# Kernel optimization log

Hardware: AMD Instinct MI355X
Metric: run time of the kernel (lower is better)

Reference implementation:

```python
import jax, jax.numpy as jnp
import numpy as np

N, D, E = 50000, 64, 800000


def setup_inputs() -> dict:
    key = jax.random.key(0)
    ks = jax.random.split(key, 12)
    scale = 1.0 / np.sqrt(D)
    inp = {
        "edge_emb_eq1": jax.random.normal(ks[0], (N, D), dtype=jnp.float32),
        "edge_index": jax.random.randint(ks[1], (2, E), 0, N, dtype=jnp.int64),
    }
    names = ["W1", "b1", "W2", "b2", "Ws", "bs", "Wmu", "bmu", "Wlv", "blv"]
    for i, name in enumerate(names):
        if name.startswith("W"):
            inp[name] = jax.random.normal(ks[2 + i], (D, D), dtype=jnp.float32) * scale
        else:
            inp[name] = jnp.zeros((D,), dtype=jnp.float32)
    return inp


def _gcn(x, W, b, src, dst, dinv):
    # GCNConv: linear transform, then symmetric-normalized aggregation with self-loops.
    x = x @ W  # [N, D]
    coef = dinv[src] * dinv[dst]                      # [E]
    msg = x[src] * coef[:, None]                      # gather + scale, [E, D]
    agg = jax.ops.segment_sum(msg, dst, num_segments=x.shape[0])  # scatter-add
    agg = agg + x * (dinv * dinv)[:, None]            # self-loop contribution
    return agg + b


def reference(edge_emb_eq1, edge_index, W1, b1, W2, b2, Ws, bs, Wmu, bmu, Wlv, blv):
    src, dst = edge_index[0], edge_index[1]
    n = edge_emb_eq1.shape[0]
    # degree (with self-loops) from destination nodes, as in PyG GCNConv
    deg = jax.ops.segment_sum(jnp.ones_like(dst, dtype=edge_emb_eq1.dtype), dst, num_segments=n) + 1.0
    dinv = jax.lax.rsqrt(deg)

    x = edge_emb_eq1
    x = _gcn(x, W1, b1, src, dst, dinv)   # encoder layer 0 (.flatten(1) is a no-op on 2D)
    x = _gcn(x, W2, b2, src, dst, dinv)   # encoder layer 1
    x = jax.nn.relu(_gcn(x, Ws, bs, src, dst, dinv))
    mu = _gcn(x, Wmu, bmu, src, dst, dinv)
    logvar = _gcn(x, Wlv, blv, src, dst, dinv)
    return (mu, logvar)
```

## Files before the change

kernel.cpp:

```cpp
#include <hip/hip_runtime.h>

#define D 64

__global__ void k_zero4(float4* __restrict__ p, int n4) {
    int i = blockIdx.x * 256 + threadIdx.x;
    if (i < n4) p[i] = make_float4(0.f, 0.f, 0.f, 0.f);
}

__global__ void k_deg(const int* __restrict__ dst, int* __restrict__ cnt8,
                      int* __restrict__ rank, int N, int E) {
    int e = blockIdx.x * 256 + threadIdx.x;
    if (e < E) rank[e] = atomicAdd(&cnt8[(size_t)(blockIdx.x & 7) * N + dst[e]], 1);
}

__global__ void k_scan1(const int* __restrict__ cnt8, int* __restrict__ part, int N) {
    __shared__ int s[256];
    int t = threadIdx.x;
    int i = blockIdx.x * 256 + t;
    int v = 0;
    if (i < N) {
        #pragma unroll
        for (int c = 0; c < 8; ++c) v += cnt8[(size_t)c * N + i];
    }
    s[t] = (v + 7) & ~7;
    __syncthreads();
    for (int d = 128; d > 0; d >>= 1) {
        if (t < d) s[t] += s[t + d];
        __syncthreads();
    }
    if (t == 0) part[blockIdx.x] = s[0];
}

__global__ void k_scan2(const int* __restrict__ part, int* __restrict__ boff, int nb) {
    __shared__ int s[256];
    int t = threadIdx.x;
    int v = (t < nb) ? part[t] : 0;
    s[t] = v;
    __syncthreads();
    for (int d = 1; d < 256; d <<= 1) {
        int add = (t >= d) ? s[t - d] : 0;
        __syncthreads();
        s[t] += add;
        __syncthreads();
    }
    if (t < nb) boff[t] = s[t] - v;
}

__global__ void k_scan3(const int* __restrict__ cnt8, const int* __restrict__ boff,
                        int* __restrict__ rp, int* __restrict__ off8,
                        float* __restrict__ dinv, int N) {
    __shared__ int s[256];
    int t = threadIdx.x;
    int i = blockIdx.x * 256 + t;
    int vc[8];
    int v = 0;
    if (i < N) {
        #pragma unroll
        for (int c = 0; c < 8; ++c) { vc[c] = cnt8[(size_t)c * N + i]; v += vc[c]; }
    }
    int pv = (v + 7) & ~7;
    s[t] = pv;
    __syncthreads();
    for (int d = 1; d < 256; d <<= 1) {
        int add = (t >= d) ? s[t - d] : 0;
        __syncthreads();
        s[t] += add;
        __syncthreads();
    }
    if (i < N) {
        int excl = boff[blockIdx.x] + s[t] - pv;
        rp[i] = excl;
        dinv[i] = 1.0f / sqrtf((float)v + 1.0f);
        int run = excl;
        #pragma unroll
        for (int c = 0; c < 8; ++c) { off8[(size_t)c * N + i] = run; run += vc[c]; }
        if (i == N - 1) rp[N] = excl + pv;
    }
}

__global__ void k_fill(const int* __restrict__ src, const int* __restrict__ dst,
                       const int* __restrict__ rank, const int* __restrict__ off8,
                       const float* __restrict__ dinv, int2* __restrict__ pack,
                       int N, int E) {
    int e = blockIdx.x * 256 + threadIdx.x;
    if (e < E) {
        int s = src[e];
        int2 p;
        p.x = s;
        p.y = __float_as_int(dinv[s]);
        pack[off8[(size_t)(blockIdx.x & 7) * N + dst[e]] + rank[e]] = p;
    }
}

template <int RELU>
__global__ __launch_bounds__(256) void k_fused(const float* __restrict__ x,
                                               const int* __restrict__ rp,
                                               const int* __restrict__ packi,
                                               const float* __restrict__ dinv,
                                               const float* __restrict__ W,
                                               const float* __restrict__ b,
                                               float* __restrict__ y, int N) {
    __shared__ float Wl[D * D];
    __shared__ float zs[16][68];
    int t = threadIdx.x;

    #pragma unroll
    for (int r = 0; r < 4; ++r) {
        float4 wv = reinterpret_cast<const float4*>(W)[t + 256 * r];
        *reinterpret_cast<float4*>(&Wl[(t + 256 * r) * 4]) = wv;
    }

    int lane = t & 63;
    int g = lane >> 4;
    int l16 = lane & 15;
    int r_loc = (t >> 6) * 4 + g;
    int n = blockIdx.x * 16 + r_loc;
    if (n < N) {
        int s0 = rp[n], s1 = rp[n + 1];
        float dn = dinv[n];
        const float4* x4 = reinterpret_cast<const float4*>(x);
        const int4* pk = reinterpret_cast<const int4*>(packi);
        float4 sv = x4[(size_t)n * 16 + l16];
        float dnn = dn * dn;
        float ax = sv.x * dnn, ay = sv.y * dnn, az = sv.z * dnn, aw = sv.w * dnn;
        float bx = 0.f, by = 0.f, bz = 0.f, bw = 0.f;
        int e = s0;
        int4 q0, q1, q2, q3;
        if (e < s1) {
            int h = e >> 1;
            q0 = pk[h]; q1 = pk[h + 1]; q2 = pk[h + 2]; q3 = pk[h + 3];
        }
        while (e < s1) {
            float4 v0 = x4[(size_t)q0.x * 16 + l16];
            float4 v1 = x4[(size_t)q0.z * 16 + l16];
            float4 v2 = x4[(size_t)q1.x * 16 + l16];
            float4 v3 = x4[(size_t)q1.z * 16 + l16];
            float4 v4 = x4[(size_t)q2.x * 16 + l16];
            float4 v5 = x4[(size_t)q2.z * 16 + l16];
            float4 v6 = x4[(size_t)q3.x * 16 + l16];
            float4 v7 = x4[(size_t)q3.z * 16 + l16];
            float c0 = __int_as_float(q0.y) * dn, c1 = __int_as_float(q0.w) * dn;
            float c2 = __int_as_float(q1.y) * dn, c3 = __int_as_float(q1.w) * dn;
            float c4 = __int_as_float(q2.y) * dn, c5 = __int_as_float(q2.w) * dn;
            float c6 = __int_as_float(q3.y) * dn, c7 = __int_as_float(q3.w) * dn;
            e += 8;
            if (e < s1) {
                int h = e >> 1;
                q0 = pk[h]; q1 = pk[h + 1]; q2 = pk[h + 2]; q3 = pk[h + 3];
            }
            ax = fmaf(v0.x, c0, ax); ay = fmaf(v0.y, c0, ay); az = fmaf(v0.z, c0, az); aw = fmaf(v0.w, c0, aw);
            bx = fmaf(v1.x, c1, bx); by = fmaf(v1.y, c1, by); bz = fmaf(v1.z, c1, bz); bw = fmaf(v1.w, c1, bw);
            ax = fmaf(v2.x, c2, ax); ay = fmaf(v2.y, c2, ay); az = fmaf(v2.z, c2, az); aw = fmaf(v2.w, c2, aw);
            bx = fmaf(v3.x, c3, bx); by = fmaf(v3.y, c3, by); bz = fmaf(v3.z, c3, bz); bw = fmaf(v3.w, c3, bw);
            ax = fmaf(v4.x, c4, ax); ay = fmaf(v4.y, c4, ay); az = fmaf(v4.z, c4, az); aw = fmaf(v4.w, c4, aw);
            bx = fmaf(v5.x, c5, bx); by = fmaf(v5.y, c5, by); bz = fmaf(v5.z, c5, bz); bw = fmaf(v5.w, c5, bw);
            ax = fmaf(v6.x, c6, ax); ay = fmaf(v6.y, c6, ay); az = fmaf(v6.z, c6, az); aw = fmaf(v6.w, c6, aw);
            bx = fmaf(v7.x, c7, bx); by = fmaf(v7.y, c7, by); bz = fmaf(v7.z, c7, bz); bw = fmaf(v7.w, c7, bw);
        }
        *reinterpret_cast<float4*>(&zs[r_loc][l16 * 4]) =
            make_float4(ax + bx, ay + by, az + bz, aw + bw);
    }
    __syncthreads();

    int col4 = (t & 15) * 4;
    int row = t >> 4;
    int nn = blockIdx.x * 16 + row;
    if (nn < N) {
        float4 acc = make_float4(0.f, 0.f, 0.f, 0.f);
        #pragma unroll
        for (int k = 0; k < D; k += 4) {
            float4 zv = *reinterpret_cast<const float4*>(&zs[row][k]);
            float4 w0 = *reinterpret_cast<const float4*>(&Wl[(k + 0) * D + col4]);
            float4 w1 = *reinterpret_cast<const float4*>(&Wl[(k + 1) * D + col4]);
            float4 w2 = *reinterpret_cast<const float4*>(&Wl[(k + 2) * D + col4]);
            float4 w3 = *reinterpret_cast<const float4*>(&Wl[(k + 3) * D + col4]);
            acc.x = fmaf(zv.x, w0.x, acc.x); acc.y = fmaf(zv.x, w0.y, acc.y);
            acc.z = fmaf(zv.x, w0.z, acc.z); acc.w = fmaf(zv.x, w0.w, acc.w);
            acc.x = fmaf(zv.y, w1.x, acc.x); acc.y = fmaf(zv.y, w1.y, acc.y);
            acc.z = fmaf(zv.y, w1.z, acc.z); acc.w = fmaf(zv.y, w1.w, acc.w);
            acc.x = fmaf(zv.z, w2.x, acc.x); acc.y = fmaf(zv.z, w2.y, acc.y);
            acc.z = fmaf(zv.z, w2.z, acc.z); acc.w = fmaf(zv.z, w2.w, acc.w);
            acc.x = fmaf(zv.w, w3.x, acc.x); acc.y = fmaf(zv.w, w3.y, acc.y);
            acc.z = fmaf(zv.w, w3.z, acc.z); acc.w = fmaf(zv.w, w3.w, acc.w);
        }
        float4 bv = *reinterpret_cast<const float4*>(&b[col4]);
        float4 r = make_float4(acc.x + bv.x, acc.y + bv.y, acc.z + bv.z, acc.w + bv.w);
        if (RELU) {
            r.x = fmaxf(r.x, 0.f); r.y = fmaxf(r.y, 0.f);
            r.z = fmaxf(r.z, 0.f); r.w = fmaxf(r.w, 0.f);
        }
        *reinterpret_cast<float4*>(&y[(size_t)nn * D + col4]) = r;
    }
}

__global__ __launch_bounds__(256) void k_fused_dual(const float* __restrict__ x,
                                                    const int* __restrict__ rp,
                                                    const int* __restrict__ packi,
                                                    const float* __restrict__ dinv,
                                                    const float* __restrict__ Wa,
                                                    const float* __restrict__ ba,
                                                    const float* __restrict__ Wb,
                                                    const float* __restrict__ bb,
                                                    float* __restrict__ ya,
                                                    float* __restrict__ yb, int N) {
    __shared__ float Wla[D * D];
    __shared__ float Wlb[D * D];
    __shared__ float zs[16][68];
    int t = threadIdx.x;

    #pragma unroll
    for (int r = 0; r < 4; ++r) {
        float4 wv = reinterpret_cast<const float4*>(Wa)[t + 256 * r];
        *reinterpret_cast<float4*>(&Wla[(t + 256 * r) * 4]) = wv;
        float4 wv2 = reinterpret_cast<const float4*>(Wb)[t + 256 * r];
        *reinterpret_cast<float4*>(&Wlb[(t + 256 * r) * 4]) = wv2;
    }

    int lane = t & 63;
    int g = lane >> 4;
    int l16 = lane & 15;
    int r_loc = (t >> 6) * 4 + g;
    int n = blockIdx.x * 16 + r_loc;
    if (n < N) {
        int s0 = rp[n], s1 = rp[n + 1];
        float dn = dinv[n];
        const float4* x4 = reinterpret_cast<const float4*>(x);
        const int4* pk = reinterpret_cast<const int4*>(packi);
        float4 sv = x4[(size_t)n * 16 + l16];
        float dnn = dn * dn;
        float ax = sv.x * dnn, ay = sv.y * dnn, az = sv.z * dnn, aw = sv.w * dnn;
        float bx = 0.f, by = 0.f, bz = 0.f, bw = 0.f;
        int e = s0;
        int4 q0, q1, q2, q3;
        if (e < s1) {
            int h = e >> 1;
            q0 = pk[h]; q1 = pk[h + 1]; q2 = pk[h + 2]; q3 = pk[h + 3];
        }
        while (e < s1) {
            float4 v0 = x4[(size_t)q0.x * 16 + l16];
            float4 v1 = x4[(size_t)q0.z * 16 + l16];
            float4 v2 = x4[(size_t)q1.x * 16 + l16];
            float4 v3 = x4[(size_t)q1.z * 16 + l16];
            float4 v4 = x4[(size_t)q2.x * 16 + l16];
            float4 v5 = x4[(size_t)q2.z * 16 + l16];
            float4 v6 = x4[(size_t)q3.x * 16 + l16];
            float4 v7 = x4[(size_t)q3.z * 16 + l16];
            float c0 = __int_as_float(q0.y) * dn, c1 = __int_as_float(q0.w) * dn;
            float c2 = __int_as_float(q1.y) * dn, c3 = __int_as_float(q1.w) * dn;
            float c4 = __int_as_float(q2.y) * dn, c5 = __int_as_float(q2.w) * dn;
            float c6 = __int_as_float(q3.y) * dn, c7 = __int_as_float(q3.w) * dn;
            e += 8;
            if (e < s1) {
                int h = e >> 1;
                q0 = pk[h]; q1 = pk[h + 1]; q2 = pk[h + 2]; q3 = pk[h + 3];
            }
            ax = fmaf(v0.x, c0, ax); ay = fmaf(v0.y, c0, ay); az = fmaf(v0.z, c0, az); aw = fmaf(v0.w, c0, aw);
            bx = fmaf(v1.x, c1, bx); by = fmaf(v1.y, c1, by); bz = fmaf(v1.z, c1, bz); bw = fmaf(v1.w, c1, bw);
            ax = fmaf(v2.x, c2, ax); ay = fmaf(v2.y, c2, ay); az = fmaf(v2.z, c2, az); aw = fmaf(v2.w, c2, aw);
            bx = fmaf(v3.x, c3, bx); by = fmaf(v3.y, c3, by); bz = fmaf(v3.z, c3, bz); bw = fmaf(v3.w, c3, bw);
            ax = fmaf(v4.x, c4, ax); ay = fmaf(v4.y, c4, ay); az = fmaf(v4.z, c4, az); aw = fmaf(v4.w, c4, aw);
            bx = fmaf(v5.x, c5, bx); by = fmaf(v5.y, c5, by); bz = fmaf(v5.z, c5, bz); bw = fmaf(v5.w, c5, bw);
            ax = fmaf(v6.x, c6, ax); ay = fmaf(v6.y, c6, ay); az = fmaf(v6.z, c6, az); aw = fmaf(v6.w, c6, aw);
            bx = fmaf(v7.x, c7, bx); by = fmaf(v7.y, c7, by); bz = fmaf(v7.z, c7, bz); bw = fmaf(v7.w, c7, bw);
        }
        *reinterpret_cast<float4*>(&zs[r_loc][l16 * 4]) =
            make_float4(ax + bx, ay + by, az + bz, aw + bw);
    }
    __syncthreads();

    int col4 = (t & 15) * 4;
    int row = t >> 4;
    int nn = blockIdx.x * 16 + row;
    if (nn < N) {
        float4 acc = make_float4(0.f, 0.f, 0.f, 0.f);
        float4 acd = make_float4(0.f, 0.f, 0.f, 0.f);
        #pragma unroll
        for (int k = 0; k < D; k += 2) {
            float z0 = zs[row][k], z1 = zs[row][k + 1];
            float4 w0 = *reinterpret_cast<const float4*>(&Wla[(k + 0) * D + col4]);
            float4 w1 = *reinterpret_cast<const float4*>(&Wla[(k + 1) * D + col4]);
            float4 u0 = *reinterpret_cast<const float4*>(&Wlb[(k + 0) * D + col4]);
            float4 u1 = *reinterpret_cast<const float4*>(&Wlb[(k + 1) * D + col4]);
            acc.x = fmaf(z0, w0.x, acc.x); acc.y = fmaf(z0, w0.y, acc.y);
            acc.z = fmaf(z0, w0.z, acc.z); acc.w = fmaf(z0, w0.w, acc.w);
            acc.x = fmaf(z1, w1.x, acc.x); acc.y = fmaf(z1, w1.y, acc.y);
            acc.z = fmaf(z1, w1.z, acc.z); acc.w = fmaf(z1, w1.w, acc.w);
            acd.x = fmaf(z0, u0.x, acd.x); acd.y = fmaf(z0, u0.y, acd.y);
            acd.z = fmaf(z0, u0.z, acd.z); acd.w = fmaf(z0, u0.w, acd.w);
            acd.x = fmaf(z1, u1.x, acd.x); acd.y = fmaf(z1, u1.y, acd.y);
            acd.z = fmaf(z1, u1.z, acd.z); acd.w = fmaf(z1, u1.w, acd.w);
        }
        float4 bav = *reinterpret_cast<const float4*>(&ba[col4]);
        float4 bbv = *reinterpret_cast<const float4*>(&bb[col4]);
        *reinterpret_cast<float4*>(&ya[(size_t)nn * D + col4]) =
            make_float4(acc.x + bav.x, acc.y + bav.y, acc.z + bav.z, acc.w + bav.w);
        *reinterpret_cast<float4*>(&yb[(size_t)nn * D + col4]) =
            make_float4(acd.x + bbv.x, acd.y + bbv.y, acd.z + bbv.z, acd.w + bbv.w);
    }
}

extern "C" void kernel_launch(void* const* d_in, const int* in_sizes, int n_in,
                              void* d_out, int out_size, void* d_ws, size_t ws_size,
                              hipStream_t stream) {
    const float* x0  = (const float*)d_in[0];
    const int*   ei  = (const int*)d_in[1];
    const float* W1  = (const float*)d_in[2];
    const float* b1  = (const float*)d_in[3];
    const float* W2  = (const float*)d_in[4];
    const float* b2  = (const float*)d_in[5];
    const float* Wsc = (const float*)d_in[6];
    const float* bs  = (const float*)d_in[7];
    const float* Wmu = (const float*)d_in[8];
    const float* bmu = (const float*)d_in[9];
    const float* Wlv = (const float*)d_in[10];
    const float* blv = (const float*)d_in[11];

    int N = in_sizes[0] / D;
    int E = in_sizes[1] / 2;
    const int* src = ei;
    const int* dst = ei + E;

    char* ws = (char*)d_ws;
    size_t off = 0;
    auto alloc = [&](size_t bytes) {
        char* p = ws + off;
        off += (bytes + 255) & ~(size_t)255;
        return p;
    };
    int*   rp   = (int*)alloc((size_t)(N + 1) * 4);
    float* dinv = (float*)alloc((size_t)N * 4);
    int NB = (N + 255) / 256;
    int* part = (int*)alloc((size_t)NB * 4);
    int* boff = (int*)alloc((size_t)NB * 4);
    int* rank = (int*)alloc((size_t)E * 4);
    int* off8 = (int*)alloc((size_t)8 * N * 4);
    char* zero_base = ws + off;
    int*  cnt8 = (int*)alloc((size_t)8 * N * 4);
    int2* pack = (int2*)alloc(((size_t)E + 8 * (size_t)N) * 8);
    size_t zero_bytes = (size_t)((char*)(pack + E + 8 * (size_t)N) - zero_base);
    int n4 = (int)((zero_bytes + 15) / 16);
    float* h1 = (float*)alloc((size_t)N * D * 4);
    float* h2 = (float*)alloc((size_t)N * D * 4);

    float* mu = (float*)d_out;
    float* lv = (float*)d_out + (size_t)N * D;

    int EB = (E + 255) / 256;
    k_zero4<<<(n4 + 255) / 256, 256, 0, stream>>>((float4*)zero_base, n4);
    k_deg  <<<EB, 256, 0, stream>>>(dst, cnt8, rank, N, E);
    k_scan1<<<NB, 256, 0, stream>>>(cnt8, part, N);
    k_scan2<<<1, 256, 0, stream>>>(part, boff, NB);
    k_scan3<<<NB, 256, 0, stream>>>(cnt8, boff, rp, off8, dinv, N);
    k_fill <<<EB, 256, 0, stream>>>(src, dst, rank, off8, dinv, pack, N, E);

    int FB = (N + 15) / 16;
    k_fused<0><<<FB, 256, 0, stream>>>(x0, rp, (const int*)pack, dinv, W1, b1, h1, N);
    k_fused<0><<<FB, 256, 0, stream>>>(h1, rp, (const int*)pack, dinv, W2, b2, h2, N);
    k_fused<1><<<FB, 256, 0, stream>>>(h2, rp, (const int*)pack, dinv, Wsc, bs, h1, N);
    k_fused_dual<<<FB, 256, 0, stream>>>(h1, rp, (const int*)pack, dinv,
                                         Wmu, bmu, Wlv, blv, mu, lv, N);
}
```

Baseline: 189.2 us.

## Drop shared-memory weight staging and block barrier; read W from global per row

Stops copying the 64x64 weight matrices into shared memory. The mini-GEMM now reads W directly from global memory, where it should stay cache resident. The block-wide __syncthreads is also removed: each row's 16 lanes, all in one wavefront, write zs and then read back only their own row, so only a wavefront-local dependency remains. This cuts LDS usage from about 20-36KB to about 4KB per block, which raises occupancy for the latency-bound gather and lets finished waves exit early. It also switches the edge-pack loads to nontemporal loads. The cost is repeated global/L1 reads of W per row and reliance on wave-synchronous LDS visibility without an explicit barrier.

```diff
diff --git a/kernel.cpp b/kernel.cpp
--- a/kernel.cpp
+++ b/kernel.cpp
@@ -1,6 +1,13 @@
 #include <hip/hip_runtime.h>
 
 #define D 64
+
+typedef int i32x4 __attribute__((ext_vector_type(4)));
+
+__device__ __forceinline__ int4 nt_load_i4(const int4* p) {
+    i32x4 v = __builtin_nontemporal_load(reinterpret_cast<const i32x4*>(p));
+    return make_int4(v.x, v.y, v.z, v.w);
+}
 
 __global__ void k_zero4(float4* __restrict__ p, int n4) {
     int i = blockIdx.x * 256 + threadIdx.x;
@@ -92,6 +99,51 @@
     }
 }
 
+__device__ __forceinline__ float4 agg_row(const float4* __restrict__ x4,
+                                          const int4* __restrict__ pk,
+                                          int s0, int s1, float dn, int n, int l16) {
+    float4 sv = x4[(size_t)n * 16 + l16];
+    float dnn = dn * dn;
+    float ax = sv.x * dnn, ay = sv.y * dnn, az = sv.z * dnn, aw = sv.w * dnn;
+    float bx = 0.f, by = 0.f, bz = 0.f, bw = 0.f;
+    int e = s0;
+    int4 q0, q1, q2, q3;
+    if (e < s1) {
+        int h = e >> 1;
+        q0 = nt_load_i4(&pk[h + 0]); q1 = nt_load_i4(&pk[h + 1]);
+        q2 = nt_load_i4(&pk[h + 2]); q3 = nt_load_i4(&pk[h + 3]);
+    }
+    while (e < s1) {
+        float4 v0 = x4[(size_t)q0.x * 16 + l16];
+        float4 v1 = x4[(size_t)q0.z * 16 + l16];
+        float4 v2 = x4[(size_t)q1.x * 16 + l16];
+        float4 v3 = x4[(size_t)q1.z * 16 + l16];
+        float4 v4 = x4[(size_t)q2.x * 16 + l16];
+        float4 v5 = x4[(size_t)q2.z * 16 + l16];
+        float4 v6 = x4[(size_t)q3.x * 16 + l16];
+        float4 v7 = x4[(size_t)q3.z * 16 + l16];
+        float c0 = __int_as_float(q0.y) * dn, c1 = __int_as_float(q0.w) * dn;
+        float c2 = __int_as_float(q1.y) * dn, c3 = __int_as_float(q1.w) * dn;
+        float c4 = __int_as_float(q2.y) * dn, c5 = __int_as_float(q2.w) * dn;
+        float c6 = __int_as_float(q3.y) * dn, c7 = __int_as_float(q3.w) * dn;
+        e += 8;
+        if (e < s1) {
+            int h = e >> 1;
+            q0 = nt_load_i4(&pk[h + 0]); q1 = nt_load_i4(&pk[h + 1]);
+            q2 = nt_load_i4(&pk[h + 2]); q3 = nt_load_i4(&pk[h + 3]);
+        }
+        ax = fmaf(v0.x, c0, ax); ay = fmaf(v0.y, c0, ay); az = fmaf(v0.z, c0, az); aw = fmaf(v0.w, c0, aw);
+        bx = fmaf(v1.x, c1, bx); by = fmaf(v1.y, c1, by); bz = fmaf(v1.z, c1, bz); bw = fmaf(v1.w, c1, bw);
+        ax = fmaf(v2.x, c2, ax); ay = fmaf(v2.y, c2, ay); az = fmaf(v2.z, c2, az); aw = fmaf(v2.w, c2, aw);
+        bx = fmaf(v3.x, c3, bx); by = fmaf(v3.y, c3, by); bz = fmaf(v3.z, c3, bz); bw = fmaf(v3.w, c3, bw);
+        ax = fmaf(v4.x, c4, ax); ay = fmaf(v4.y, c4, ay); az = fmaf(v4.z, c4, az); aw = fmaf(v4.w, c4, aw);
+        bx = fmaf(v5.x, c5, bx); by = fmaf(v5.y, c5, by); bz = fmaf(v5.z, c5, bz); bw = fmaf(v5.w, c5, bw);
+        ax = fmaf(v6.x, c6, ax); ay = fmaf(v6.y, c6, ay); az = fmaf(v6.z, c6, az); aw = fmaf(v6.w, c6, aw);
+        bx = fmaf(v7.x, c7, bx); by = fmaf(v7.y, c7, by); bz = fmaf(v7.z, c7, bz); bw = fmaf(v7.w, c7, bw);
+    }
+    return make_float4(ax + bx, ay + by, az + bz, aw + bw);
+}
+
 template <int RELU>
 __global__ __launch_bounds__(256) void k_fused(const float* __restrict__ x,
                                                const int* __restrict__ rp,
@@ -100,97 +152,45 @@
                                                const float* __restrict__ W,
                                                const float* __restrict__ b,
                                                float* __restrict__ y, int N) {
-    __shared__ float Wl[D * D];
     __shared__ float zs[16][68];
     int t = threadIdx.x;
-
-    #pragma unroll
-    for (int r = 0; r < 4; ++r) {
-        float4 wv = reinterpret_cast<const float4*>(W)[t + 256 * r];
-        *reinterpret_cast<float4*>(&Wl[(t + 256 * r) * 4]) = wv;
-    }
-
     int lane = t & 63;
     int g = lane >> 4;
     int l16 = lane & 15;
     int r_loc = (t >> 6) * 4 + g;
     int n = blockIdx.x * 16 + r_loc;
-    if (n < N) {
-        int s0 = rp[n], s1 = rp[n + 1];
-        float dn = dinv[n];
-        const float4* x4 = reinterpret_cast<const float4*>(x);
-        const int4* pk = reinterpret_cast<const int4*>(packi);
-        float4 sv = x4[(size_t)n * 16 + l16];
-        float dnn = dn * dn;
-        float ax = sv.x * dnn, ay = sv.y * dnn, az = sv.z * dnn, aw = sv.w * dnn;
-        float bx = 0.f, by = 0.f, bz = 0.f, bw = 0.f;
-        int e = s0;
-        int4 q0, q1, q2, q3;
-        if (e < s1) {
-            int h = e >> 1;
-            q0 = pk[h]; q1 = pk[h + 1]; q2 = pk[h + 2]; q3 = pk[h + 3];
-        }
-        while (e < s1) {
-            float4 v0 = x4[(size_t)q0.x * 16 + l16];
-            float4 v1 = x4[(size_t)q0.z * 16 + l16];
-            float4 v2 = x4[(size_t)q1.x * 16 + l16];
-            float4 v3 = x4[(size_t)q1.z * 16 + l16];
-            float4 v4 = x4[(size_t)q2.x * 16 + l16];
-            float4 v5 = x4[(size_t)q2.z * 16 + l16];
-            float4 v6 = x4[(size_t)q3.x * 16 + l16];
-            float4 v7 = x4[(size_t)q3.z * 16 + l16];
-            float c0 = __int_as_float(q0.y) * dn, c1 = __int_as_float(q0.w) * dn;
-            float c2 = __int_as_float(q1.y) * dn, c3 = __int_as_float(q1.w) * dn;
-            float c4 = __int_as_float(q2.y) * dn, c5 = __int_as_float(q2.w) * dn;
-            float c6 = __int_as_float(q3.y) * dn, c7 = __int_as_float(q3.w) * dn;
-            e += 8;
-            if (e < s1) {
-                int h = e >> 1;
-                q0 = pk[h]; q1 = pk[h + 1]; q2 = pk[h + 2]; q3 = pk[h + 3];
-            }
-            ax = fmaf(v0.x, c0, ax); ay = fmaf(v0.y, c0, ay); az = fmaf(v0.z, c0, az); aw = fmaf(v0.w, c0, aw);
-            bx = fmaf(v1.x, c1, bx); by = fmaf(v1.y, c1, by); bz = fmaf(v1.z, c1, bz); bw = fmaf(v1.w, c1, bw);
-            ax = fmaf(v2.x, c2, ax); ay = fmaf(v2.y, c2, ay); az = fmaf(v2.z, c2, az); aw = fmaf(v2.w, c2, aw);
-            bx = fmaf(v3.x, c3, bx); by = fmaf(v3.y, c3, by); bz = fmaf(v3.z, c3, bz); bw = fmaf(v3.w, c3, bw);
-            ax = fmaf(v4.x, c4, ax); ay = fmaf(v4.y, c4, ay); az = fmaf(v4.z, c4, az); aw = fmaf(v4.w, c4, aw);
-            bx = fmaf(v5.x, c5, bx); by = fmaf(v5.y, c5, by); bz = fmaf(v5.z, c5, bz); bw = fmaf(v5.w, c5, bw);
-            ax = fmaf(v6.x, c6, ax); ay = fmaf(v6.y, c6, ay); az = fmaf(v6.z, c6, az); aw = fmaf(v6.w, c6, aw);
-            bx = fmaf(v7.x, c7, bx); by = fmaf(v7.y, c7, by); bz = fmaf(v7.z, c7, bz); bw = fmaf(v7.w, c7, bw);
-        }
-        *reinterpret_cast<float4*>(&zs[r_loc][l16 * 4]) =
-            make_float4(ax + bx, ay + by, az + bz, aw + bw);
-    }
-    __syncthreads();
-
-    int col4 = (t & 15) * 4;
-    int row = t >> 4;
-    int nn = blockIdx.x * 16 + row;
-    if (nn < N) {
-        float4 acc = make_float4(0.f, 0.f, 0.f, 0.f);
-        #pragma unroll
-        for (int k = 0; k < D; k += 4) {
-            float4 zv = *reinterpret_cast<const float4*>(&zs[row][k]);
-            float4 w0 = *reinterpret_cast<const float4*>(&Wl[(k + 0) * D + col4]);
-            float4 w1 = *reinterpret_cast<const float4*>(&Wl[(k + 1) * D + col4]);
-            float4 w2 = *reinterpret_cast<const float4*>(&Wl[(k + 2) * D + col4]);
-            float4 w3 = *reinterpret_cast<const float4*>(&Wl[(k + 3) * D + col4]);
-            acc.x = fmaf(zv.x, w0.x, acc.x); acc.y = fmaf(zv.x, w0.y, acc.y);
-            acc.z = fmaf(zv.x, w0.z, acc.z); acc.w = fmaf(zv.x, w0.w, acc.w);
-            acc.x = fmaf(zv.y, w1.x, acc.x); acc.y = fmaf(zv.y, w1.y, acc.y);
-            acc.z = fmaf(zv.y, w1.z, acc.z); acc.w = fmaf(zv.y, w1.w, acc.w);
-            acc.x = fmaf(zv.z, w2.x, acc.x); acc.y = fmaf(zv.z, w2.y, acc.y);
-            acc.z = fmaf(zv.z, w2.z, acc.z); acc.w = fmaf(zv.z, w2.w, acc.w);
-            acc.x = fmaf(zv.w, w3.x, acc.x); acc.y = fmaf(zv.w, w3.y, acc.y);
-            acc.z = fmaf(zv.w, w3.z, acc.z); acc.w = fmaf(zv.w, w3.w, acc.w);
-        }
-        float4 bv = *reinterpret_cast<const float4*>(&b[col4]);
-        float4 r = make_float4(acc.x + bv.x, acc.y + bv.y, acc.z + bv.z, acc.w + bv.w);
-        if (RELU) {
-            r.x = fmaxf(r.x, 0.f); r.y = fmaxf(r.y, 0.f);
-            r.z = fmaxf(r.z, 0.f); r.w = fmaxf(r.w, 0.f);
-        }
-        *reinterpret_cast<float4*>(&y[(size_t)nn * D + col4]) = r;
-    }
+    if (n >= N) return;
+
+    float4 z = agg_row(reinterpret_cast<const float4*>(x),
+                       reinterpret_cast<const int4*>(packi),
+                       rp[n], rp[n + 1], dinv[n], n, l16);
+    *reinterpret_cast<float4*>(&zs[r_loc][l16 * 4]) = z;
+
+    int col4 = l16 * 4;
+    float4 acc = make_float4(0.f, 0.f, 0.f, 0.f);
+    #pragma unroll 4
+    for (int k = 0; k < D; k += 4) {
+        float4 zv = *reinterpret_cast<const float4*>(&zs[r_loc][k]);
+        float4 w0 = *reinterpret_cast<const float4*>(&W[(k + 0) * D + col4]);
+        float4 w1 = *reinterpret_cast<const float4*>(&W[(k + 1) * D + col4]);
+        float4 w2 = *reinterpret_cast<const float4*>(&W[(k + 2) * D + col4]);
+        float4 w3 = *reinterpret_cast<const float4*>(&W[(k + 3) * D + col4]);
+        acc.x = fmaf(zv.x, w0.x, acc.x); acc.y = fmaf(zv.x, w0.y, acc.y);
+        acc.z = fmaf(zv.x, w0.z, acc.z); acc.w = fmaf(zv.x, w0.w, acc.w);
+        acc.x = fmaf(zv.y, w1.x, acc.x); acc.y = fmaf(zv.y, w1.y, acc.y);
+        acc.z = fmaf(zv.y, w1.z, acc.z); acc.w = fmaf(zv.y, w1.w, acc.w);
+        acc.x = fmaf(zv.z, w2.x, acc.x); acc.y = fmaf(zv.z, w2.y, acc.y);
+        acc.z = fmaf(zv.z, w2.z, acc.z); acc.w = fmaf(zv.z, w2.w, acc.w);
+        acc.x = fmaf(zv.w, w3.x, acc.x); acc.y = fmaf(zv.w, w3.y, acc.y);
+        acc.z = fmaf(zv.w, w3.z, acc.z); acc.w = fmaf(zv.w, w3.w, acc.w);
+    }
+    float4 bv = *reinterpret_cast<const float4*>(&b[col4]);
+    float4 r = make_float4(acc.x + bv.x, acc.y + bv.y, acc.z + bv.z, acc.w + bv.w);
+    if (RELU) {
+        r.x = fmaxf(r.x, 0.f); r.y = fmaxf(r.y, 0.f);
+        r.z = fmaxf(r.z, 0.f); r.w = fmaxf(r.w, 0.f);
+    }
+    *reinterpret_cast<float4*>(&y[(size_t)n * D + col4]) = r;
 }
 
 __global__ __launch_bounds__(256) void k_fused_dual(const float* __restrict__ x,
@@ -203,100 +203,45 @@
                                                     const float* __restrict__ bb,
                                                     float* __restrict__ ya,
                                                     float* __restrict__ yb, int N) {
-    __shared__ float Wla[D * D];
-    __shared__ float Wlb[D * D];
     __shared__ float zs[16][68];
     int t = threadIdx.x;
-
-    #pragma unroll
-    for (int r = 0; r < 4; ++r) {
-        float4 wv = reinterpret_cast<const float4*>(Wa)[t + 256 * r];
-        *reinterpret_cast<float4*>(&Wla[(t + 256 * r) * 4]) = wv;
-        float4 wv2 = reinterpret_cast<const float4*>(Wb)[t + 256 * r];
-        *reinterpret_cast<float4*>(&Wlb[(t + 256 * r) * 4]) = wv2;
-    }
-
     int lane = t & 63;
     int g = lane >> 4;
     int l16 = lane & 15;
     int r_loc = (t >> 6) * 4 + g;
     int n = blockIdx.x * 16 + r_loc;
-    if (n < N) {
-        int s0 = rp[n], s1 = rp[n + 1];
-        float dn = dinv[n];
-        const float4* x4 = reinterpret_cast<const float4*>(x);
-        const int4* pk = reinterpret_cast<const int4*>(packi);
-        float4 sv = x4[(size_t)n * 16 + l16];
-        float dnn = dn * dn;
-        float ax = sv.x * dnn, ay = sv.y * dnn, az = sv.z * dnn, aw = sv.w * dnn;
-        float bx = 0.f, by = 0.f, bz = 0.f, bw = 0.f;
-        int e = s0;
-        int4 q0, q1, q2, q3;
-        if (e < s1) {
-            int h = e >> 1;
-            q0 = pk[h]; q1 = pk[h + 1]; q2 = pk[h + 2]; q3 = pk[h + 3];
-        }
-        while (e < s1) {
-            float4 v0 = x4[(size_t)q0.x * 16 + l16];
-            float4 v1 = x4[(size_t)q0.z * 16 + l16];
-            float4 v2 = x4[(size_t)q1.x * 16 + l16];
-            float4 v3 = x4[(size_t)q1.z * 16 + l16];
-            float4 v4 = x4[(size_t)q2.x * 16 + l16];
-            float4 v5 = x4[(size_t)q2.z * 16 + l16];
-            float4 v6 = x4[(size_t)q3.x * 16 + l16];
-            float4 v7 = x4[(size_t)q3.z * 16 + l16];
-            float c0 = __int_as_float(q0.y) * dn, c1 = __int_as_float(q0.w) * dn;
-            float c2 = __int_as_float(q1.y) * dn, c3 = __int_as_float(q1.w) * dn;
-            float c4 = __int_as_float(q2.y) * dn, c5 = __int_as_float(q2.w) * dn;
-            float c6 = __int_as_float(q3.y) * dn, c7 = __int_as_float(q3.w) * dn;
-            e += 8;
-            if (e < s1) {
-                int h = e >> 1;
-                q0 = pk[h]; q1 = pk[h + 1]; q2 = pk[h + 2]; q3 = pk[h + 3];
-            }
-            ax = fmaf(v0.x, c0, ax); ay = fmaf(v0.y, c0, ay); az = fmaf(v0.z, c0, az); aw = fmaf(v0.w, c0, aw);
-            bx = fmaf(v1.x, c1, bx); by = fmaf(v1.y, c1, by); bz = fmaf(v1.z, c1, bz); bw = fmaf(v1.w, c1, bw);
-            ax = fmaf(v2.x, c2, ax); ay = fmaf(v2.y, c2, ay); az = fmaf(v2.z, c2, az); aw = fmaf(v2.w, c2, aw);
-            bx = fmaf(v3.x, c3, bx); by = fmaf(v3.y, c3, by); bz = fmaf(v3.z, c3, bz); bw = fmaf(v3.w, c3, bw);
-            ax = fmaf(v4.x, c4, ax); ay = fmaf(v4.y, c4, ay); az = fmaf(v4.z, c4, az); aw = fmaf(v4.w, c4, aw);
-            bx = fmaf(v5.x, c5, bx); by = fmaf(v5.y, c5, by); bz = fmaf(v5.z, c5, bz); bw = fmaf(v5.w, c5, bw);
-            ax = fmaf(v6.x, c6, ax); ay = fmaf(v6.y, c6, ay); az = fmaf(v6.z, c6, az); aw = fmaf(v6.w, c6, aw);
-            bx = fmaf(v7.x, c7, bx); by = fmaf(v7.y, c7, by); bz = fmaf(v7.z, c7, bz); bw = fmaf(v7.w, c7, bw);
-        }
-        *reinterpret_cast<float4*>(&zs[r_loc][l16 * 4]) =
-            make_float4(ax + bx, ay + by, az + bz, aw + bw);
-    }
-    __syncthreads();
-
-    int col4 = (t & 15) * 4;
-    int row = t >> 4;
-    int nn = blockIdx.x * 16 + row;
-    if (nn < N) {
-        float4 acc = make_float4(0.f, 0.f, 0.f, 0.f);
-        float4 acd = make_float4(0.f, 0.f, 0.f, 0.f);
-        #pragma unroll
-        for (int k = 0; k < D; k += 2) {
-            float z0 = zs[row][k], z1 = zs[row][k + 1];
-            float4 w0 = *reinterpret_cast<const float4*>(&Wla[(k + 0) * D + col4]);
-            float4 w1 = *reinterpret_cast<const float4*>(&Wla[(k + 1) * D + col4]);
-            float4 u0 = *reinterpret_cast<const float4*>(&Wlb[(k + 0) * D + col4]);
-            float4 u1 = *reinterpret_cast<const float4*>(&Wlb[(k + 1) * D + col4]);
-            acc.x = fmaf(z0, w0.x, acc.x); acc.y = fmaf(z0, w0.y, acc.y);
-            acc.z = fmaf(z0, w0.z, acc.z); acc.w = fmaf(z0, w0.w, acc.w);
-            acc.x = fmaf(z1, w1.x, acc.x); acc.y = fmaf(z1, w1.y, acc.y);
-            acc.z = fmaf(z1, w1.z, acc.z); acc.w = fmaf(z1, w1.w, acc.w);
-            acd.x = fmaf(z0, u0.x, acd.x); acd.y = fmaf(z0, u0.y, acd.y);
-            acd.z = fmaf(z0, u0.z, acd.z); acd.w = fmaf(z0, u0.w, acd.w);
-            acd.x = fmaf(z1, u1.x, acd.x); acd.y = fmaf(z1, u1.y, acd.y);
-            acd.z = fmaf(z1, u1.z, acd.z); acd.w = fmaf(z1, u1.w, acd.w);
-        }
-        float4 bav = *reinterpret_cast<const float4*>(&ba[col4]);
-        float4 bbv = *reinterpret_cast<const float4*>(&bb[col4]);
-        *reinterpret_cast<float4*>(&ya[(size_t)nn * D + col4]) =
-            make_float4(acc.x + bav.x, acc.y + bav.y, acc.z + bav.z, acc.w + bav.w);
-        *reinterpret_cast<float4*>(&yb[(size_t)nn * D + col4]) =
-            make_float4(acd.x + bbv.x, acd.y + bbv.y, acd.z + bbv.z, acd.w + bbv.w);
-    }
+    if (n >= N) return;
+
+    float4 z = agg_row(reinterpret_cast<const float4*>(x),
+                       reinterpret_cast<const int4*>(packi),
+                       rp[n], rp[n + 1], dinv[n], n, l16);
+    *reinterpret_cast<float4*>(&zs[r_loc][l16 * 4]) = z;
+
+    int col4 = l16 * 4;
+    float4 acc = make_float4(0.f, 0.f, 0.f, 0.f);
+    float4 acd = make_float4(0.f, 0.f, 0.f, 0.f);
+    #pragma unroll 4
+    for (int k = 0; k < D; k += 2) {
+        float z0 = zs[r_loc][k], z1 = zs[r_loc][k + 1];
+        float4 w0 = *reinterpret_cast<const float4*>(&Wa[(k + 0) * D + col4]);
+        float4 w1 = *reinterpret_cast<const float4*>(&Wa[(k + 1) * D + col4]);
+        float4 u0 = *reinterpret_cast<const float4*>(&Wb[(k + 0) * D + col4]);
+        float4 u1 = *reinterpret_cast<const float4*>(&Wb[(k + 1) * D + col4]);
+        acc.x = fmaf(z0, w0.x, acc.x); acc.y = fmaf(z0, w0.y, acc.y);
+        acc.z = fmaf(z0, w0.z, acc.z); acc.w = fmaf(z0, w0.w, acc.w);
+        acc.x = fmaf(z1, w1.x, acc.x); acc.y = fmaf(z1, w1.y, acc.y);
+        acc.z = fmaf(z1, w1.z, acc.z); acc.w = fmaf(z1, w1.w, acc.w);
+        acd.x = fmaf(z0, u0.x, acd.x); acd.y = fmaf(z0, u0.y, acd.y);
+        acd.z = fmaf(z0, u0.z, acd.z); acd.w = fmaf(z0, u0.w, acd.w);
+        acd.x = fmaf(z1, u1.x, acd.x); acd.y = fmaf(z1, u1.y, acd.y);
+        acd.z = fmaf(z1, u1.z, acd.z); acd.w = fmaf(z1, u1.w, acd.w);
+    }
+    float4 bav = *reinterpret_cast<const float4*>(&ba[col4]);
+    float4 bbv = *reinterpret_cast<const float4*>(&bb[col4]);
+    *reinterpret_cast<float4*>(&ya[(size_t)n * D + col4]) =
+        make_float4(acc.x + bav.x, acc.y + bav.y, acc.z + bav.z, acc.w + bav.w);
+    *reinterpret_cast<float4*>(&yb[(size_t)n * D + col4]) =
+        make_float4(acd.x + bbv.x, acd.y + bbv.y, acd.z + bbv.z, acd.w + bbv.w);
 }
 
 extern "C" void kernel_launch(void* const* d_in, const int* in_sizes, int n_in,
```

After: 274.5 us. +45.1%, slower.
